# Kernel optimization log

Measured on AMD Instinct MI355X. Metric: run time of the kernel, lower is better.

Reference implementation:

```python
import jax, jax.numpy as jnp
import numpy as np

D_MODEL, D_K, D_V, N_HEADS = 1024, 64, 64, 16
B, S = 4, 4096
LN_EPS = 1e-5
NORM_EPS = 1e-12  # torch F.normalize default eps


def setup_inputs() -> dict:
    key = jax.random.key(0)
    ks = jax.random.split(key, 9)
    s = 0.02
    return {
        "x": jax.random.normal(ks[0], (B, S, D_MODEL), dtype=jnp.float32),
        # nn.Linear weights have shape [out, in]
        "W_Q": jax.random.normal(ks[1], (N_HEADS * D_K, D_MODEL), dtype=jnp.float32) * s,
        "W_K": jax.random.normal(ks[2], (N_HEADS * D_K, D_MODEL), dtype=jnp.float32) * s,
        "W_V": jax.random.normal(ks[3], (N_HEADS * D_V, D_MODEL), dtype=jnp.float32) * s,
        "W_g": jax.random.normal(ks[4], (N_HEADS * D_V, D_MODEL), dtype=jnp.float32) * s,
        "W_alpha": jax.random.normal(ks[5], (N_HEADS, D_MODEL), dtype=jnp.float32) * s,
        "W_O": jax.random.normal(ks[6], (D_MODEL, N_HEADS * D_V), dtype=jnp.float32) * s,
        "ln_gamma": jnp.ones((D_MODEL,), dtype=jnp.float32),
        "ln_beta": jnp.zeros((D_MODEL,), dtype=jnp.float32),
    }


def reference(x, W_Q, W_K, W_V, W_g, W_alpha, W_O, ln_gamma, ln_beta):
    # --- input projection chain (unfused variant) ---
    Q_raw = jnp.einsum('bsd,od->bso', x, W_Q)               # [B,S,H*Dk] (unused downstream)
    K_raw = jnp.einsum('bsd,od->bso', x, W_K)               # [B,S,H*Dk]
    V = jnp.einsum('bsd,od->bso', x, W_V)                   # [B,S,H*Dv]
    g_raw = jnp.einsum('bsd,od->bso', x, W_g)               # [B,S,H*Dv]
    alpha_raw = jnp.einsum('bsd,od->bso', x, W_alpha)       # [B,S,H]

    # F.normalize over the full last dim (n_heads*d_k), eps clamp on the norm
    K_norm = K_raw / jnp.maximum(jnp.linalg.norm(K_raw, axis=-1, keepdims=True), NORM_EPS)
    gate = jax.nn.silu(g_raw)
    alpha = jax.nn.sigmoid(alpha_raw)

    # scan is simulated as identity: scan_output = V
    scan_output = V

    # --- output epilogue: gate-multiply + output GEMM + residual + LayerNorm ---
    gated = scan_output * gate
    projected = jnp.einsum('bsv,dv->bsd', gated, W_O)
    pre = projected + x
    mean = jnp.mean(pre, axis=-1, keepdims=True)
    var = jnp.mean(jnp.square(pre - mean), axis=-1, keepdims=True)
    out = (pre - mean) * jax.lax.rsqrt(var + LN_EPS) * ln_gamma + ln_beta
    return out
```

## Files before the change

### kernel.cpp

```cpp
#include <hip/hip_runtime.h>

#define M_TOT 16384
#define DM    1024

typedef unsigned short ushort_t;
typedef __bf16 bf16x8 __attribute__((ext_vector_type(8)));
typedef float  f32x4  __attribute__((ext_vector_type(4)));

__device__ __forceinline__ ushort_t f32_to_bf16(float f) {
    union { float f; unsigned u; } v; v.f = f;
    unsigned u = v.u;
    return (ushort_t)((u + 0x7fffu + ((u >> 16) & 1u)) >> 16);
}
__device__ __forceinline__ float bf16_to_f32(ushort_t h) {
    union { unsigned u; float f; } v; v.u = ((unsigned)h) << 16;
    return v.f;
}

__device__ __forceinline__ void gload16(const ushort_t* g, ushort_t* l) {
    __builtin_amdgcn_global_load_lds(
        (const __attribute__((address_space(1))) unsigned int*)g,
        (__attribute__((address_space(3))) unsigned int*)l,
        16, 0, 0);
}

__global__ __launch_bounds__(256) void cvt_all(const float* __restrict__ x,
                                               const float* __restrict__ wv,
                                               const float* __restrict__ wg,
                                               const float* __restrict__ wo,
                                               ushort_t* __restrict__ xb,
                                               ushort_t* __restrict__ wcat,
                                               ushort_t* __restrict__ wob) {
    const long NX = (long)M_TOT * DM / 4, NW = (long)DM * DM / 4;
    long i = (long)blockIdx.x * 256 + threadIdx.x;
    const float* src; ushort_t* dst; long so, di;
    if (i < NX) {
        src = x; so = i; dst = xb; di = i;
    } else if (i < NX + NW) {
        long j = i - NX; src = wv; so = j;
        int row = (int)(j >> 8), c4 = (int)(j & 255);
        int orow = ((row >> 4) << 5) | (row & 15);
        dst = wcat; di = (long)orow * 256 + c4;
    } else if (i < NX + 2 * NW) {
        long j = i - NX - NW; src = wg; so = j;
        int row = (int)(j >> 8), c4 = (int)(j & 255);
        int orow = ((row >> 4) << 5) | 16 | (row & 15);
        dst = wcat; di = (long)orow * 256 + c4;
    } else {
        long j = i - NX - 2 * NW; src = wo; so = j; dst = wob; di = j;
    }
    const float4 v = ((const float4*)src)[so];
    ushort4 o;
    o.x = f32_to_bf16(v.x); o.y = f32_to_bf16(v.y);
    o.z = f32_to_bf16(v.z); o.w = f32_to_bf16(v.w);
    ((ushort4*)dst)[di] = o;
}

template<int EPI>
__global__ __launch_bounds__(512, 2) void gemmS(
    const ushort_t* __restrict__ A,
    const ushort_t* __restrict__ Bm,
    const ushort_t* __restrict__ Xb,
    ushort_t* __restrict__ out,
    int nbs)
{
    extern __shared__ ushort_t lds[];

    const int flat = blockIdx.x;
    const int xcd  = flat & 7;
    const int ii   = flat >> 3;
    const int m0   = ((xcd << 3) + (ii >> nbs)) << 8;
    const int n0   = (ii & ((1 << nbs) - 1)) << 8;

    const int tid  = threadIdx.x;
    const int w    = tid >> 6;
    const int l    = tid & 63;
    const int wm   = w >> 2;
    const int wn   = w & 3;
    const int fr   = l & 15;
    const int quad = l >> 4;

    f32x4 acc[8][4];
    const f32x4 vzero = {0.f, 0.f, 0.f, 0.f};
#pragma unroll
    for (int i = 0; i < 8; ++i)
#pragma unroll
        for (int j = 0; j < 4; ++j) acc[i][j] = vzero;

    const long sA0 = (long)(m0 + w * 16 + fr) * DM + (quad << 3);
    const long sA1 = sA0 + 128 * (long)DM;
    const long sB0 = (long)(n0 + w * 16 + fr) * DM + (quad << 3);
    const long sB1 = sB0 + 128 * (long)DM;

    auto stageA = [&](int u) {
        const int d  = (u & 3) * 16384 + w * 512;
        const int ko = u * 32;
        gload16(A + sA0 + ko, lds + d);
        gload16(A + sA1 + ko, lds + d + 4096);
    };
    auto stageB = [&](int u) {
        const int d  = (u & 3) * 16384 + 8192 + w * 512;
        const int ko = u * 32;
        gload16(Bm + sB0 + ko, lds + d);
        gload16(Bm + sB1 + ko, lds + d + 4096);
    };

    const int rA = wm * 4096 + l * 8;
    const int rB = 8192 + wn * 2048 + l * 8;

    stageA(0); stageB(0);
    stageA(1); stageB(1);
    stageA(2); stageB(2);
    asm volatile("s_waitcnt vmcnt(8)" ::: "memory");
    __builtin_amdgcn_s_barrier();

    for (int u = 0; u < 32; ++u) {
        const int sb = (u & 3) * 16384;
        bf16x8 af[4], bf[4];

#pragma unroll
        for (int j = 0; j < 4; ++j) bf[j] = *(const bf16x8*)(lds + sb + rB + j * 512);
#pragma unroll
        for (int i = 0; i < 4; ++i) af[i] = *(const bf16x8*)(lds + sb + rA + i * 512);
        if (u < 29) stageA(u + 3);
        __builtin_amdgcn_s_barrier();
        __builtin_amdgcn_s_setprio(1);
#pragma unroll
        for (int j = 0; j < 4; ++j)
#pragma unroll
            for (int i = 0; i < 4; ++i)
                acc[i][j] = __builtin_amdgcn_mfma_f32_16x16x32_bf16(
                    af[i], bf[j], acc[i][j], 0, 0, 0);
        __builtin_amdgcn_s_setprio(0);
        __builtin_amdgcn_s_barrier();

#pragma unroll
        for (int i = 0; i < 4; ++i) af[i] = *(const bf16x8*)(lds + sb + rA + (4 + i) * 512);
        if (u < 29) stageB(u + 3);
        __builtin_amdgcn_s_barrier();
        __builtin_amdgcn_s_setprio(1);
#pragma unroll
        for (int j = 0; j < 4; ++j)
#pragma unroll
            for (int i = 0; i < 4; ++i)
                acc[4 + i][j] = __builtin_amdgcn_mfma_f32_16x16x32_bf16(
                    af[i], bf[j], acc[4 + i][j], 0, 0, 0);
        __builtin_amdgcn_s_setprio(0);
        if (u < 29)       { asm volatile("s_waitcnt vmcnt(8)" ::: "memory"); }
        else if (u == 29) { asm volatile("s_waitcnt vmcnt(4)" ::: "memory"); }
        else if (u == 30) { asm volatile("s_waitcnt vmcnt(0)" ::: "memory"); }
        __builtin_amdgcn_sched_barrier(0);
        __builtin_amdgcn_s_barrier();
    }

    const int rowb = m0 + wm * 128;
    const int colb = n0 + wn * 64;
    if (EPI == 0) {
#pragma unroll
        for (int i = 0; i < 8; ++i)
#pragma unroll
            for (int jp = 0; jp < 2; ++jp) {
                const int cb   = colb + jp * 32;
                const int vcol = ((cb >> 5) << 4) + fr;
#pragma unroll
                for (int r = 0; r < 4; ++r) {
                    const int row = rowb + i * 16 + quad * 4 + r;
                    float v = acc[i][2 * jp][r];
                    float g = acc[i][2 * jp + 1][r];
                    float gate = g / (1.0f + __expf(-g));
                    out[(long)row * DM + vcol] = f32_to_bf16(v * gate);
                }
            }
    } else {
#pragma unroll
        for (int i = 0; i < 8; ++i)
#pragma unroll
            for (int j = 0; j < 4; ++j) {
                const int col = colb + j * 16 + fr;
#pragma unroll
                for (int r = 0; r < 4; ++r) {
                    const int row = rowb + i * 16 + quad * 4 + r;
                    float pre = acc[i][j][r] + bf16_to_f32(Xb[(long)row * DM + col]);
                    out[(long)row * DM + col] = f32_to_bf16(pre);
                }
            }
    }
}

__global__ __launch_bounds__(256) void ln_rows(const ushort_t* __restrict__ pre,
                                               const float* __restrict__ gamma,
                                               const float* __restrict__ beta,
                                               float* __restrict__ out)
{
    const int row = blockIdx.x;
    const int tid = threadIdx.x;
    const int wave = tid >> 6, lane = tid & 63;

    ushort4 u = ((const ushort4*)(pre + row * DM))[tid];
    float p0 = bf16_to_f32(u.x), p1 = bf16_to_f32(u.y);
    float p2 = bf16_to_f32(u.z), p3 = bf16_to_f32(u.w);

    float s  = p0 + p1 + p2 + p3;
    float ss = p0 * p0 + p1 * p1 + p2 * p2 + p3 * p3;
#pragma unroll
    for (int off = 32; off > 0; off >>= 1) {
        s  += __shfl_down(s, off);
        ss += __shfl_down(ss, off);
    }
    __shared__ float red[8];
    __shared__ float mb[2];
    if (lane == 0) { red[wave] = s; red[4 + wave] = ss; }
    __syncthreads();
    if (tid == 0) {
        float S  = red[0] + red[1] + red[2] + red[3];
        float SS = red[4] + red[5] + red[6] + red[7];
        float mean = S * (1.0f / 1024.0f);
        float var  = SS * (1.0f / 1024.0f) - mean * mean;
        mb[0] = mean;
        mb[1] = rsqrtf(var + 1e-5f);
    }
    __syncthreads();
    const float mean = mb[0], rs = mb[1];

    float4 gm = ((const float4*)gamma)[tid];
    float4 bt = ((const float4*)beta)[tid];
    float4 o;
    o.x = (p0 - mean) * rs * gm.x + bt.x;
    o.y = (p1 - mean) * rs * gm.y + bt.y;
    o.z = (p2 - mean) * rs * gm.z + bt.z;
    o.w = (p3 - mean) * rs * gm.w + bt.w;
    ((float4*)(out + row * DM))[tid] = o;
}

extern "C" void kernel_launch(void* const* d_in, const int* in_sizes, int n_in,
                              void* d_out, int out_size, void* d_ws, size_t ws_size,
                              hipStream_t stream) {
    const float* x     = (const float*)d_in[0];
    const float* WV    = (const float*)d_in[3];
    const float* WG    = (const float*)d_in[4];
    const float* WO    = (const float*)d_in[6];
    const float* gamma = (const float*)d_in[7];
    const float* beta  = (const float*)d_in[8];
    float* out = (float*)d_out;

    char* ws = (char*)d_ws;
    ushort_t* xb    = (ushort_t*)ws;
    ushort_t* gated = (ushort_t*)(ws + (size_t)M_TOT * DM * 2);
    ushort_t* wcat  = (ushort_t*)(ws + (size_t)M_TOT * DM * 4);
    ushort_t* wob   = (ushort_t*)(ws + (size_t)M_TOT * DM * 4 + (size_t)2 * DM * DM * 2);
    ushort_t* pre   = xb;

    static bool attr_set = false;
    if (!attr_set) {
        hipFuncSetAttribute((const void*)&gemmS<0>,
                            hipFuncAttributeMaxDynamicSharedMemorySize, 131072);
        hipFuncSetAttribute((const void*)&gemmS<1>,
                            hipFuncAttributeMaxDynamicSharedMemorySize, 131072);
        attr_set = true;
    }

    const int nCvt = (M_TOT * DM + 3 * DM * DM) / 4 / 256;
    cvt_all<<<nCvt, 256, 0, stream>>>(x, WV, WG, WO, xb, wcat, wob);

    gemmS<0><<<512, 512, 131072, stream>>>(xb, wcat, nullptr, gated, 3);
    gemmS<1><<<256, 512, 131072, stream>>>(gated, wob, xb, pre, 2);

    ln_rows<<<M_TOT, 256, 0, stream>>>(pre, gamma, beta, out);
}
```

Baseline: 270.4 us.

## Store GEMM operands in K-panel-major layout for contiguous tile loads

Converts x, the concatenated V/gate weights and W_O into a K-blocked layout where each 32-wide K slice of all rows is contiguous. The GEMM staging loads, the gated-output store and the residual read all use this panel layout. Each K-step's tile load then reads one contiguous chunk instead of 16-byte pieces at a 2 KB row stride, which aims to improve DRAM/TLB locality. The cost is strided scatter writes in the conversion kernel and epilogue, which now write 2-byte elements 64 bytes apart. The pre-LN buffer also moves to its own workspace region instead of reusing xb.

Measured after the change: 269.5 us. No clear change (-0.4%).

```diff
diff --git a/kernel.cpp b/kernel.cpp
--- a/kernel.cpp
+++ b/kernel.cpp
@@ -28,26 +28,34 @@
                                                const float* __restrict__ wv,
                                                const float* __restrict__ wg,
                                                const float* __restrict__ wo,
-                                               ushort_t* __restrict__ xb,
+                                               ushort_t* __restrict__ xkt,
                                                ushort_t* __restrict__ wcat,
                                                ushort_t* __restrict__ wob) {
     const long NX = (long)M_TOT * DM / 4, NW = (long)DM * DM / 4;
     long i = (long)blockIdx.x * 256 + threadIdx.x;
     const float* src; ushort_t* dst; long so, di;
     if (i < NX) {
-        src = x; so = i; dst = xb; di = i;
+        src = x; so = i;
+        int row = (int)(i >> 8), col0 = (int)(i & 255) << 2;
+        dst = xkt;
+        di = ((long)(col0 >> 5) * M_TOT + row) * 8 + ((col0 & 31) >> 2);
     } else if (i < NX + NW) {
         long j = i - NX; src = wv; so = j;
-        int row = (int)(j >> 8), c4 = (int)(j & 255);
+        int row = (int)(j >> 8), col0 = (int)(j & 255) << 2;
         int orow = ((row >> 4) << 5) | (row & 15);
-        dst = wcat; di = (long)orow * 256 + c4;
+        dst = wcat;
+        di = ((long)(col0 >> 5) * 2048 + orow) * 8 + ((col0 & 31) >> 2);
     } else if (i < NX + 2 * NW) {
         long j = i - NX - NW; src = wg; so = j;
-        int row = (int)(j >> 8), c4 = (int)(j & 255);
+        int row = (int)(j >> 8), col0 = (int)(j & 255) << 2;
         int orow = ((row >> 4) << 5) | 16 | (row & 15);
-        dst = wcat; di = (long)orow * 256 + c4;
+        dst = wcat;
+        di = ((long)(col0 >> 5) * 2048 + orow) * 8 + ((col0 & 31) >> 2);
     } else {
-        long j = i - NX - 2 * NW; src = wo; so = j; dst = wob; di = j;
+        long j = i - NX - 2 * NW; src = wo; so = j;
+        int row = (int)(j >> 8), col0 = (int)(j & 255) << 2;
+        dst = wob;
+        di = ((long)(col0 >> 5) * 1024 + row) * 8 + ((col0 & 31) >> 2);
     }
     const float4 v = ((const float4*)src)[so];
     ushort4 o;
@@ -56,12 +64,12 @@
     ((ushort4*)dst)[di] = o;
 }
 
-template<int EPI>
+template<int EPI, int NB>
 __global__ __launch_bounds__(512, 2) void gemmS(
     const ushort_t* __restrict__ A,
     const ushort_t* __restrict__ Bm,
     const ushort_t* __restrict__ Xb,
-    ushort_t* __restrict__ out,
+    ushort_t* __restrict__ out0,
     int nbs)
 {
     extern __shared__ ushort_t lds[];
@@ -87,22 +95,20 @@
 #pragma unroll
         for (int j = 0; j < 4; ++j) acc[i][j] = vzero;
 
-    const long sA0 = (long)(m0 + w * 16 + fr) * DM + (quad << 3);
-    const long sA1 = sA0 + 128 * (long)DM;
-    const long sB0 = (long)(n0 + w * 16 + fr) * DM + (quad << 3);
-    const long sB1 = sB0 + 128 * (long)DM;
+    const int sA = (m0 + w * 16 + fr) * 32 + (quad << 3);
+    const int sB = (n0 + w * 16 + fr) * 32 + (quad << 3);
 
     auto stageA = [&](int u) {
-        const int d  = (u & 3) * 16384 + w * 512;
-        const int ko = u * 32;
-        gload16(A + sA0 + ko, lds + d);
-        gload16(A + sA1 + ko, lds + d + 4096);
+        const int  d  = (u & 3) * 16384 + w * 512;
+        const long po = (long)u * (M_TOT * 32);
+        gload16(A + po + sA, lds + d);
+        gload16(A + po + sA + 4096, lds + d + 4096);
     };
     auto stageB = [&](int u) {
-        const int d  = (u & 3) * 16384 + 8192 + w * 512;
-        const int ko = u * 32;
-        gload16(Bm + sB0 + ko, lds + d);
-        gload16(Bm + sB1 + ko, lds + d + 4096);
+        const int  d  = (u & 3) * 16384 + 8192 + w * 512;
+        const long po = (long)u * (NB * 32);
+        gload16(Bm + po + sB, lds + d);
+        gload16(Bm + po + sB + 4096, lds + d + 4096);
     };
 
     const int rA = wm * 4096 + l * 8;
@@ -162,13 +168,14 @@
             for (int jp = 0; jp < 2; ++jp) {
                 const int cb   = colb + jp * 32;
                 const int vcol = ((cb >> 5) << 4) + fr;
+                const long kbase = ((long)(vcol >> 5) * M_TOT) * 32 + (vcol & 31);
 #pragma unroll
                 for (int r = 0; r < 4; ++r) {
                     const int row = rowb + i * 16 + quad * 4 + r;
                     float v = acc[i][2 * jp][r];
                     float g = acc[i][2 * jp + 1][r];
                     float gate = g / (1.0f + __expf(-g));
-                    out[(long)row * DM + vcol] = f32_to_bf16(v * gate);
+                    out0[kbase + (long)row * 32] = f32_to_bf16(v * gate);
                 }
             }
     } else {
@@ -177,11 +184,12 @@
 #pragma unroll
             for (int j = 0; j < 4; ++j) {
                 const int col = colb + j * 16 + fr;
+                const long xbase = ((long)(col >> 5) * M_TOT) * 32 + (col & 31);
 #pragma unroll
                 for (int r = 0; r < 4; ++r) {
                     const int row = rowb + i * 16 + quad * 4 + r;
-                    float pre = acc[i][j][r] + bf16_to_f32(Xb[(long)row * DM + col]);
-                    out[(long)row * DM + col] = f32_to_bf16(pre);
+                    float pre = acc[i][j][r] + bf16_to_f32(Xb[xbase + (long)row * 32]);
+                    out0[(long)row * DM + col] = f32_to_bf16(pre);
                 }
             }
     }
@@ -196,7 +204,7 @@
     const int tid = threadIdx.x;
     const int wave = tid >> 6, lane = tid & 63;
 
-    ushort4 u = ((const ushort4*)(pre + row * DM))[tid];
+    ushort4 u = ((const ushort4*)(pre + (long)row * DM))[tid];
     float p0 = bf16_to_f32(u.x), p1 = bf16_to_f32(u.y);
     float p2 = bf16_to_f32(u.z), p3 = bf16_to_f32(u.w);
 
@@ -229,7 +237,7 @@
     o.y = (p1 - mean) * rs * gm.y + bt.y;
     o.z = (p2 - mean) * rs * gm.z + bt.z;
     o.w = (p3 - mean) * rs * gm.w + bt.w;
-    ((float4*)(out + row * DM))[tid] = o;
+    ((float4*)(out + (long)row * DM))[tid] = o;
 }
 
 extern "C" void kernel_launch(void* const* d_in, const int* in_sizes, int n_in,
@@ -243,27 +251,29 @@
     const float* beta  = (const float*)d_in[8];
     float* out = (float*)d_out;
 
+    const size_t SZX = (size_t)M_TOT * DM * 2;
+    const size_t SZW = (size_t)DM * DM * 2;
     char* ws = (char*)d_ws;
-    ushort_t* xb    = (ushort_t*)ws;
-    ushort_t* gated = (ushort_t*)(ws + (size_t)M_TOT * DM * 2);
-    ushort_t* wcat  = (ushort_t*)(ws + (size_t)M_TOT * DM * 4);
-    ushort_t* wob   = (ushort_t*)(ws + (size_t)M_TOT * DM * 4 + (size_t)2 * DM * DM * 2);
-    ushort_t* pre   = xb;
+    ushort_t* xkt   = (ushort_t*)ws;
+    ushort_t* gated = (ushort_t*)(ws + SZX);
+    ushort_t* wcat  = (ushort_t*)(ws + 2 * SZX);
+    ushort_t* wob   = (ushort_t*)(ws + 2 * SZX + 2 * SZW);
+    ushort_t* pre   = (ushort_t*)(ws + 2 * SZX + 3 * SZW);
 
     static bool attr_set = false;
     if (!attr_set) {
-        hipFuncSetAttribute((const void*)&gemmS<0>,
+        hipFuncSetAttribute((const void*)&gemmS<0, 2048>,
                             hipFuncAttributeMaxDynamicSharedMemorySize, 131072);
-        hipFuncSetAttribute((const void*)&gemmS<1>,
+        hipFuncSetAttribute((const void*)&gemmS<1, 1024>,
                             hipFuncAttributeMaxDynamicSharedMemorySize, 131072);
         attr_set = true;
     }
 
     const int nCvt = (M_TOT * DM + 3 * DM * DM) / 4 / 256;
-    cvt_all<<<nCvt, 256, 0, stream>>>(x, WV, WG, WO, xb, wcat, wob);
-
-    gemmS<0><<<512, 512, 131072, stream>>>(xb, wcat, nullptr, gated, 3);
-    gemmS<1><<<256, 512, 131072, stream>>>(gated, wob, xb, pre, 2);
+    cvt_all<<<nCvt, 256, 0, stream>>>(x, WV, WG, WO, xkt, wcat, wob);
+
+    gemmS<0, 2048><<<512, 512, 131072, stream>>>(xkt, wcat, nullptr, gated, 3);
+    gemmS<1, 1024><<<256, 512, 131072, stream>>>(gated, wob, xkt, pre, 2);
 
     ln_rows<<<M_TOT, 256, 0, stream>>>(pre, gamma, beta, out);
 }
```
